# Kernel tuning notes

Hardware: AMD Instinct MI355X
Metric: run time of the kernel (lower is better)

Reference implementation:

```python
import jax, jax.numpy as jnp
import numpy as np

B, S, D_MODEL = 2, 2048, 768
N_QK, D_QK = 16, 16
N_OV, D_OV = 256, 1
VKV = 16
ROT_DIM, ROT_BASE = 16, 10000.0
SCALE = D_QK ** 0.5  # attn_scale defaults to sqrt(d_qk_head)


def _rotary_sin_cos(n_ctx, rotary_dim, base):
    # TransformerLens-style, non-adjacent pairs (GPT-NeoX)
    pos = jnp.arange(n_ctx, dtype=jnp.float32)
    dim = jnp.arange(rotary_dim // 2, dtype=jnp.float32)
    freq = base ** (dim / (rotary_dim / 2))
    freq = jnp.concatenate([freq, freq])  # 'd -> (2 d)'
    angles = pos[:, None] / freq[None, :]  # [n_ctx, rotary_dim]
    return jnp.sin(angles), jnp.cos(angles)


def _apply_rotary(x, sin, cos):
    # x: [B, S, H, d_head]; rotate first ROT_DIM dims, pass through the rest
    s = x.shape[1]
    xr = x[..., :ROT_DIM]
    half = ROT_DIM // 2
    rot = jnp.concatenate([-xr[..., half:], xr[..., :half]], axis=-1)  # rotate_every_two (non-adjacent)
    xr = xr * cos[:s, None, :] + rot * sin[:s, None, :]
    return jnp.concatenate([xr, x[..., ROT_DIM:]], axis=-1) if x.shape[-1] > ROT_DIM else xr


def setup_inputs() -> dict:
    key = jax.random.key(0)
    ks = jax.random.split(key, 6)
    std_qk = np.sqrt(2.0 / (D_MODEL * D_QK))   # kaiming fan_in for [H, d_model, d_head]
    std_v = np.sqrt(2.0 / (D_MODEL * D_OV))
    std_o = np.sqrt(2.0 / (D_OV * D_MODEL))
    std_vk = np.sqrt(2.0 / (N_QK * D_QK))
    return {
        "resid": jax.random.normal(ks[0], (B, S, D_MODEL), jnp.float32),
        "W_Q": jax.random.normal(ks[1], (N_QK, D_MODEL, D_QK), jnp.float32) * std_qk,
        "W_K": jax.random.normal(ks[2], (N_QK, D_MODEL, D_QK), jnp.float32) * std_qk,
        "W_V": jax.random.normal(ks[3], (N_OV, D_MODEL, D_OV), jnp.float32) * std_v,
        "W_O": jax.random.normal(ks[4], (N_OV, D_OV, D_MODEL), jnp.float32) * std_o,
        "b_Q": jnp.zeros((N_QK, D_QK), jnp.float32),
        "b_K": jnp.zeros((N_QK, D_QK), jnp.float32),
        "b_V": jnp.zeros((N_OV, D_OV), jnp.float32),
        "b_O": jnp.zeros((D_MODEL,), jnp.float32),
        "virtual_k": jax.random.normal(ks[5], (VKV, N_QK, D_QK), jnp.float32) * std_vk,
        "virtual_v": jnp.zeros((VKV, N_OV, D_OV), jnp.float32),
    }


def reference(resid, W_Q, W_K, W_V, W_O, b_Q, b_K, b_V, b_O, virtual_k, virtual_v):
    b, s, _ = resid.shape
    sin, cos = _rotary_sin_cos(s, ROT_DIM, ROT_BASE)

    q = jnp.einsum('bsd,hde->bshe', resid, W_Q) + b_Q  # [B,S,N_QK,D_QK]
    k = jnp.einsum('bsd,hde->bshe', resid, W_K) + b_K
    v = jnp.einsum('bsd,hde->bshe', resid, W_V) + b_V  # [B,S,N_OV,1]

    q = _apply_rotary(q, sin, cos)
    k = _apply_rotary(k, sin, cos)

    # append virtual KV along key axis
    k = jnp.concatenate([k, jnp.broadcast_to(virtual_k[None], (b, VKV, N_QK, D_QK))], axis=1)
    v = jnp.concatenate([v, jnp.broadcast_to(virtual_v[None], (b, VKV, N_OV, D_OV))], axis=1)

    scores = jnp.einsum('bqhe,bkhe->bhqk', q, k) / SCALE  # [B,H,S,S+VKV]
    i = jnp.arange(s)[:, None]
    j = jnp.arange(s + VKV)[None, :]
    mask = (j - i) <= VKV  # tril(.., diagonal=VKV)
    scores = jnp.where(mask, scores, -jnp.inf)
    pattern = jax.nn.softmax(scores, axis=-1)
    pattern = jnp.where(jnp.isnan(pattern), 0.0, pattern)

    r = N_OV // N_QK
    v_r = v.transpose(0, 2, 1, 3).reshape(b, N_QK, r, s + VKV, D_OV)  # [B,n_qk,r,K,1]
    z = jnp.einsum('bnqk,bnrkh->bnrqh', pattern, v_r)  # [B,n_qk,r,S,1]
    z = z.reshape(b, N_OV, s, D_OV).transpose(0, 2, 1, 3)  # [B,S,N_OV,1]

    out = jnp.einsum('bqhd,hdm->bqm', z, W_O) + b_O  # [B,S,D_MODEL]
    return out
```

## Files before the change

kernel.cpp:

```cpp
#include <hip/hip_runtime.h>
#include <hip/hip_bf16.h>
#include <math.h>

#define B_   2
#define S_   2048
#define DM   768
#define H_   16
#define C_   256
#define VKV_ 16
#define SK   2064
#define SKP  2080
#define NT_  65

#define TSPLIT 16
#define MAXSP  5
#define NACT   164

typedef __attribute__((ext_vector_type(8))) short short8;
typedef __attribute__((ext_vector_type(4))) short short4v;
typedef __attribute__((ext_vector_type(4))) float f32x4;
typedef __attribute__((ext_vector_type(16))) float f32x16;
typedef __attribute__((ext_vector_type(4))) unsigned uint4v;

#define QSCALE 0.360673760222240851f
#define L2B8   1.6609640474436811f

__device__ __forceinline__ short tobf(float f) {
    union { float f; unsigned u; } x; x.f = f;
    unsigned r = x.u + 0x7FFFu + ((x.u >> 16) & 1u);
    return (short)(r >> 16);
}
__device__ __forceinline__ float frombf_lo(unsigned u) {
    union { unsigned u; float f; } x; x.u = u << 16; return x.f;
}
__device__ __forceinline__ float frombf_hi(unsigned u) {
    union { unsigned u; float f; } x; x.u = u & 0xFFFF0000u; return x.f;
}

__device__ __forceinline__ void gload_lds16(const short* g, short* l) {
    __builtin_amdgcn_global_load_lds(
        (const __attribute__((address_space(1))) unsigned int*)g,
        (__attribute__((address_space(3))) unsigned int*)l, 16, 0, 0);
}

#define NRES (4096*768/4)
#define NWQ  (768*768)
#define NWO  (768*256)
__global__ __launch_bounds__(256) void conv_all(
    const float* __restrict__ resid,
    const float* __restrict__ WQ, const float* __restrict__ WK,
    const float* __restrict__ WV, const float* __restrict__ WO,
    const float* __restrict__ bQ, const float* __restrict__ bK,
    const float* __restrict__ bV,
    const float* __restrict__ vKp, const float* __restrict__ vVp,
    short* __restrict__ Ab, short* __restrict__ Wqkv_t,
    short* __restrict__ WtO, float* __restrict__ bqkv,
    short* __restrict__ Kb2, short* __restrict__ Vt3)
{
    int t = blockIdx.x * 256 + threadIdx.x;
    if (t < NRES) {
        float4 v = *(const float4*)(resid + (size_t)t * 4);
        short4v o = { tobf(v.x), tobf(v.y), tobf(v.z), tobf(v.w) };
        *(short4v*)(Ab + (size_t)t * 4) = o;
        return;
    }
    t -= NRES;
    if (t < NWQ) {
        int cc = t / 768, d = t % 768;
        float w;
        if (cc < 256)      w = WQ[((size_t)(cc >> 4) * DM + d) * 16 + (cc & 15)];
        else if (cc < 512) w = WK[((size_t)((cc - 256) >> 4) * DM + d) * 16 + (cc & 15)];
        else               w = WV[(size_t)(cc - 512) * DM + d];
        Wqkv_t[t] = tobf(w);
        return;
    }
    t -= NWQ;
    if (t < NWO) {
        int c = t & 255, m = t >> 8;
        WtO[t] = tobf(WO[(size_t)c * DM + m]);
        return;
    }
    t -= NWO;
    if (t < 768) {
        bqkv[t] = (t < 256) ? bQ[t] : (t < 512 ? bK[t - 256] : bV[t - 512]);
        return;
    }
    t -= 768;
    if (t < 32 * 32) {
        const int bh = t >> 5;
        const int s  = S_ + (t & 31);
        const int h  = bh & 15;
        short kb[16], vb[16];
        if (s < SK) {
            const int tt = s - S_;
#pragma unroll
            for (int e = 0; e < 16; ++e) {
                kb[e] = tobf(vKp[(size_t)tt * 256 + h * 16 + e]);
                vb[e] = tobf(vVp[(size_t)tt * 256 + h * 16 + e]);
            }
        } else {
#pragma unroll
            for (int e = 0; e < 16; ++e) { kb[e] = 0; vb[e] = 0; }
        }
        const int t5 = s >> 5;
        short* kbase = Kb2 + ((size_t)bh * NT_ + t5) * 512 + (s & 31) * 8;
#pragma unroll
        for (int e = 0; e < 8; ++e)  { kbase[e] = kb[e]; kbase[256 + e] = kb[e + 8]; }
        short* vbase = Vt3 + ((size_t)bh * NT_ + t5) * 1024
                     + ((s >> 4) & 1) * 512 + ((s >> 3) & 1) * 8 + (s & 7);
#pragma unroll
        for (int dv = 0; dv < 16; ++dv) vbase[dv * 16] = vb[dv];
    }
}

__global__ __launch_bounds__(256) void mm_qkv(
    const short* __restrict__ A, const short* __restrict__ Bt,
    const float* __restrict__ bias,
    short* __restrict__ Qb2, short* __restrict__ Kb2, short* __restrict__ Vt3)
{
    __shared__ short As[128 * 64];
    __shared__ short Bs[64 * 64];

    const int tid  = threadIdx.x;
    const int w    = tid >> 6;
    const int lane = tid & 63;
    const int wm   = w >> 1, wn = w & 1;
    const int g    = lane >> 4, c = lane & 15;
    const int m0   = blockIdx.y * 128;
    const int n0   = blockIdx.x * 64;

    f32x4 acc[4][2];
#pragma unroll
    for (int i = 0; i < 4; ++i)
#pragma unroll
        for (int j = 0; j < 2; ++j) acc[i][j] = (f32x4){0.f, 0.f, 0.f, 0.f};

    const int lr = lane >> 3;
    const int lc = lane & 7;

    for (int k0 = 0; k0 < 768; k0 += 64) {
#pragma unroll
        for (int i = 0; i < 4; ++i) {
            const int ch  = i * 4 + w;
            const int row = ch * 8 + lr;
            const int scc = lc ^ (row & 7);
            gload_lds16(A + (size_t)(m0 + row) * 768 + k0 + scc * 8, As + ch * 512);
        }
#pragma unroll
        for (int i = 0; i < 2; ++i) {
            const int ch  = i * 4 + w;
            const int row = ch * 8 + lr;
            const int scc = lc ^ (row & 7);
            gload_lds16(Bt + (size_t)(n0 + row) * 768 + k0 + scc * 8, Bs + ch * 512);
        }
        __syncthreads();
#pragma unroll
        for (int kk = 0; kk < 64; kk += 32) {
            short8 af[4], bf[2];
#pragma unroll
            for (int i = 0; i < 4; ++i) {
                const int row = wm * 64 + i * 16 + c;
                const int sc  = ((kk >> 3) + g) ^ (row & 7);
                af[i] = *(const short8*)(As + row * 64 + sc * 8);
            }
#pragma unroll
            for (int j = 0; j < 2; ++j) {
                const int row = wn * 32 + j * 16 + c;
                const int sc  = ((kk >> 3) + g) ^ (row & 7);
                bf[j] = *(const short8*)(Bs + row * 64 + sc * 8);
            }
#pragma unroll
            for (int i = 0; i < 4; ++i)
#pragma unroll
                for (int j = 0; j < 2; ++j)
                    acc[i][j] = __builtin_amdgcn_mfma_f32_16x16x32_bf16(
                        af[i], bf[j], acc[i][j], 0, 0, 0);
        }
        __syncthreads();
    }

    const float bv0 = bias[n0 + wn * 32 + c];
    const float bv1 = bias[n0 + wn * 32 + 16 + c];

    if (n0 < 512) {
        const int isQ = (n0 < 256) ? 1 : 0;
        const float invf = __builtin_amdgcn_exp2f(-(float)(c & 7) * L2B8);
        const int h0 = (((n0 + wn * 32) & 255) >> 4);
        const int elo = (c & 8) ? 0 : 1;
#pragma unroll
        for (int i = 0; i < 4; ++i) {
#pragma unroll
            for (int r = 0; r < 4; ++r) {
                const int row = m0 + wm * 64 + i * 16 + 4 * g + r;
                const int s   = row & 2047;
                const int b   = row >> 11;
                float sn, cs;
                __sincosf((float)s * invf, &sn, &cs);
#pragma unroll
                for (int j = 0; j < 2; ++j) {
                    float val = acc[i][j][r] + (j ? bv1 : bv0);
                    float par = __shfl_xor(val, 8);
                    float rot = elo ? -par : par;
                    float out = val * cs + rot * sn;
                    if (isQ) out *= QSCALE;
                    const int bh = b * 16 + h0 + j;
                    const size_t base = isQ
                        ? ((size_t)bh * 64 + (s >> 5)) * 512
                        : ((size_t)bh * NT_ + (s >> 5)) * 512;
                    short* dst = (isQ ? Qb2 : Kb2) + base
                               + (s & 31) * 8 + (c >> 3) * 256 + (c & 7);
                    *dst = tobf(out);
                }
            }
        }
    } else {
        const int h0 = ((n0 + wn * 32 - 512) >> 4);
#pragma unroll
        for (int i = 0; i < 4; ++i) {
#pragma unroll
            for (int r = 0; r < 4; ++r) {
                const int row = m0 + wm * 64 + i * 16 + 4 * g + r;
                const int s   = row & 2047;
                const int b   = row >> 11;
#pragma unroll
                for (int j = 0; j < 2; ++j) {
                    float val = acc[i][j][r] + (j ? bv1 : bv0);
                    const int bh = b * 16 + h0 + j;
                    short* dst = Vt3 + ((size_t)bh * NT_ + (s >> 5)) * 1024
                               + ((s >> 4) & 1) * 512 + ((s >> 3) & 1) * 8 + (s & 7)
                               + c * 16;
                    *dst = tobf(val);
                }
            }
        }
    }
}

__global__ __launch_bounds__(256) void mm_out(
    const short* __restrict__ A, const short* __restrict__ Bt,
    const float* __restrict__ bias, float* __restrict__ Cout)
{
    __shared__ short As[128 * 64];
    __shared__ short Bs[64 * 64];

    const int tid  = threadIdx.x;
    const int w    = tid >> 6;
    const int lane = tid & 63;
    const int wm   = w >> 1, wn = w & 1;
    const int g    = lane >> 4, c = lane & 15;
    const int m0   = blockIdx.y * 128;
    const int n0   = blockIdx.x * 64;

    f32x4 acc[4][2];
#pragma unroll
    for (int i = 0; i < 4; ++i)
#pragma unroll
        for (int j = 0; j < 2; ++j) acc[i][j] = (f32x4){0.f, 0.f, 0.f, 0.f};

    const int lr = lane >> 3;
    const int lc = lane & 7;

    for (int k0 = 0; k0 < 256; k0 += 64) {
#pragma unroll
        for (int i = 0; i < 4; ++i) {
            const int ch  = i * 4 + w;
            const int row = ch * 8 + lr;
            const int scc = lc ^ (row & 7);
            gload_lds16(A + (size_t)(m0 + row) * 256 + k0 + scc * 8, As + ch * 512);
        }
#pragma unroll
        for (int i = 0; i < 2; ++i) {
            const int ch  = i * 4 + w;
            const int row = ch * 8 + lr;
            const int scc = lc ^ (row & 7);
            gload_lds16(Bt + (size_t)(n0 + row) * 256 + k0 + scc * 8, Bs + ch * 512);
        }
        __syncthreads();
#pragma unroll
        for (int kk = 0; kk < 64; kk += 32) {
            short8 af[4], bf[2];
#pragma unroll
            for (int i = 0; i < 4; ++i) {
                const int row = wm * 64 + i * 16 + c;
                const int sc  = ((kk >> 3) + g) ^ (row & 7);
                af[i] = *(const short8*)(As + row * 64 + sc * 8);
            }
#pragma unroll
            for (int j = 0; j < 2; ++j) {
                const int row = wn * 32 + j * 16 + c;
                const int sc  = ((kk >> 3) + g) ^ (row & 7);
                bf[j] = *(const short8*)(Bs + row * 64 + sc * 8);
            }
#pragma unroll
            for (int i = 0; i < 4; ++i)
#pragma unroll
                for (int j = 0; j < 2; ++j)
                    acc[i][j] = __builtin_amdgcn_mfma_f32_16x16x32_bf16(
                        af[i], bf[j], acc[i][j], 0, 0, 0);
        }
        __syncthreads();
    }
#pragma unroll
    for (int i = 0; i < 4; ++i)
#pragma unroll
        for (int j = 0; j < 2; ++j) {
            const int col = n0 + wn * 32 + j * 16 + c;
            const float bv = bias[col];
#pragma unroll
            for (int r = 0; r < 4; ++r) {
                const int row = m0 + wm * 64 + i * 16 + 4 * g + r;
                Cout[(size_t)row * DM + col] = acc[i][j][r] + bv;
            }
        }
}

__global__ __launch_bounds__(256) void attn_split(
    const short* __restrict__ Qb2, const short* __restrict__ Kb2,
    const short* __restrict__ Vt3, unsigned* __restrict__ PartA,
    float* __restrict__ PartL)
{
    const int w    = threadIdx.x >> 6;
    const int lane = threadIdx.x & 63;
    const int blk  = blockIdx.x;
    const int xcd  = blk & 7;
    const int j    = blk >> 3;
    const int bhl  = j / 41;
    const int slot = j - bhl * 41;
    const int bh   = xcd * 4 + bhl;
    const int r    = slot * 4 + w;
    int qt, sp;
    if (r < 49)       { sp = 1; qt = 15 + r; }
    else if (r < 82)  { sp = 2; qt = 31 + (r - 49); }
    else if (r < 99)  { sp = 3; qt = 47 + (r - 82); }
    else if (r == 99) { sp = 4; qt = 63; }
    else              { sp = 0; qt = 163 - r; }

    const int nt   = qt + 2;
    const int t0   = sp * TSPLIT;
    const int tend = min(t0 + TSPLIT, nt);

    const int hi = lane >> 5;
    const int qc = lane & 31;
    const int q0 = qt * 32;

    const f32x16 zero16 = {0,0,0,0,0,0,0,0,0,0,0,0,0,0,0,0};

    short8 qf = *(const short8*)(Qb2 + ((size_t)bh * 64 + qt) * 512 + lane * 8);

    f32x16 acc = zero16;
    float lsum = 0.f;

    const short* kbase = Kb2 + (size_t)bh * NT_ * 512 + lane * 8;
    const short* vbase = Vt3 + (size_t)bh * NT_ * 1024 + (lane & 15) * 16 + hi * 8;
    const int qv16  = q0 + qc + 16;
    const int tmask = (q0 + 17) >> 5;

#define LK(tt)  (*(const short8*)(kbase + (size_t)(tt) * 512))
#define LVA(tt) (*(const short8*)(vbase + (size_t)(tt) * 1024))
#define LVB(tt) (*(const short8*)(vbase + (size_t)(tt) * 1024 + 512))

#define SOFTMAX_TILE(S, tt, B1, B2)                                          \
    {                                                                        \
        if ((tt) >= tmask) {                                                 \
            const int kt_ = (tt) * 32;                                       \
            _Pragma("unroll")                                                \
            for (int rr = 0; rr < 16; ++rr) {                                \
                const int key = kt_ + (rr & 3) + 8 * (rr >> 2) + 4 * hi;     \
                S[rr] = (key <= qv16) ? S[rr] : -INFINITY;                   \
            }                                                                \
        }                                                                    \
        unsigned pk[8];                                                      \
        _Pragma("unroll")                                                    \
        for (int jj = 0; jj < 8; ++jj) {                                     \
            const float p0 = __builtin_amdgcn_exp2f(S[2 * jj]);              \
            const float p1 = __builtin_amdgcn_exp2f(S[2 * jj + 1]);          \
            lsum += p0 + p1;                                                 \
            asm("v_cvt_pk_bf16_f32 %0, %1, %2" : "=v"(pk[jj]) : "v"(p0), "v"(p1)); \
        }                                                                    \
        unsigned a0 = pk[0], a2 = pk[2], a1 = pk[1], a3 = pk[3];             \
        unsigned a4 = pk[4], a6 = pk[6], a5 = pk[5], a7 = pk[7];             \
        asm("v_permlane32_swap_b32 %0, %1" : "+v"(a0), "+v"(a2));            \
        asm("v_permlane32_swap_b32 %0, %1" : "+v"(a1), "+v"(a3));            \
        asm("v_permlane32_swap_b32 %0, %1" : "+v"(a4), "+v"(a6));            \
        asm("v_permlane32_swap_b32 %0, %1" : "+v"(a5), "+v"(a7));            \
        B1.u[0] = a0; B1.u[1] = a1; B1.u[2] = a2; B1.u[3] = a3;              \
        B2.u[0] = a4; B2.u[1] = a5; B2.u[2] = a6; B2.u[3] = a7;              \
    }

    const int npair_end = t0 + ((tend - t0) & ~1);

    if (t0 < npair_end) {
        short8 kfA = LK(t0),     vaA = LVA(t0),     vvA = LVB(t0);
        short8 kfB = LK(t0 + 1), vaB = LVA(t0 + 1), vvB = LVB(t0 + 1);

        for (int t = t0; t < npair_end; t += 2) {
            short8 kfA_n = kfA, vaA_n = vaA, vvA_n = vvA;
            short8 kfB_n = kfB, vaB_n = vaB, vvB_n = vvB;
            if (t + 2 < npair_end) {
                kfA_n = LK(t + 2); vaA_n = LVA(t + 2); vvA_n = LVB(t + 2);
                kfB_n = LK(t + 3); vaB_n = LVA(t + 3); vvB_n = LVB(t + 3);
            }

            f32x16 S0 = __builtin_amdgcn_mfma_f32_32x32x16_bf16(kfA, qf, zero16, 0, 0, 0);
            f32x16 S1 = __builtin_amdgcn_mfma_f32_32x32x16_bf16(kfB, qf, zero16, 0, 0, 0);

            union { unsigned u[4]; short8 v; } b1A, b2A, b1B, b2B;
            SOFTMAX_TILE(S0, t,     b1A, b2A);
            SOFTMAX_TILE(S1, t + 1, b1B, b2B);

            acc = __builtin_amdgcn_mfma_f32_32x32x16_bf16(vaA, b1A.v, acc, 0, 0, 0);
            acc = __builtin_amdgcn_mfma_f32_32x32x16_bf16(vvA, b2A.v, acc, 0, 0, 0);
            acc = __builtin_amdgcn_mfma_f32_32x32x16_bf16(vaB, b1B.v, acc, 0, 0, 0);
            acc = __builtin_amdgcn_mfma_f32_32x32x16_bf16(vvB, b2B.v, acc, 0, 0, 0);

            kfA = kfA_n; vaA = vaA_n; vvA = vvA_n;
            kfB = kfB_n; vaB = vaB_n; vvB = vvB_n;
        }
    }
    if (npair_end < tend) {
        const int t = npair_end;
        short8 kf = LK(t), va = LVA(t), vv = LVB(t);
        f32x16 S0 = __builtin_amdgcn_mfma_f32_32x32x16_bf16(kf, qf, zero16, 0, 0, 0);
        union { unsigned u[4]; short8 v; } b1, b2;
        SOFTMAX_TILE(S0, t, b1, b2);
        acc = __builtin_amdgcn_mfma_f32_32x32x16_bf16(va, b1.v, acc, 0, 0, 0);
        acc = __builtin_amdgcn_mfma_f32_32x32x16_bf16(vv, b2.v, acc, 0, 0, 0);
    }

    uint4v pa;
    asm("v_cvt_pk_bf16_f32 %0, %1, %2" : "=v"(pa.x) : "v"(acc[0]), "v"(acc[1]));
    asm("v_cvt_pk_bf16_f32 %0, %1, %2" : "=v"(pa.y) : "v"(acc[2]), "v"(acc[3]));
    asm("v_cvt_pk_bf16_f32 %0, %1, %2" : "=v"(pa.z) : "v"(acc[4]), "v"(acc[5]));
    asm("v_cvt_pk_bf16_f32 %0, %1, %2" : "=v"(pa.w) : "v"(acc[6]), "v"(acc[7]));

    const int pidx = (bh * 64 + qt) * MAXSP + sp;
    *(uint4v*)(PartA + ((size_t)pidx * 64 + lane) * 4) = pa;

    lsum += __shfl_xor(lsum, 32);
    if (hi == 0) PartL[(size_t)pidx * 32 + qc] = lsum;
}

__global__ __launch_bounds__(256) void attn_combine(
    const unsigned* __restrict__ PartA, const float* __restrict__ PartL,
    short* __restrict__ Zb)
{
    const int w    = threadIdx.x >> 6;
    const int lane = threadIdx.x & 63;
    const int wid  = blockIdx.x * 4 + w;
    const int bh   = wid >> 6;
    const int qt   = wid & 63;
    const int hi   = lane >> 5;
    const int qc   = lane & 31;
    const int ns   = (qt + 2 + TSPLIT - 1) / TSPLIT;

    float a[8];
#pragma unroll
    for (int rr = 0; rr < 8; ++rr) a[rr] = 0.f;
    float lsum = 0.f;

    const int pbase = (bh * 64 + qt) * MAXSP;
    for (int sp = 0; sp < ns; ++sp) {
        uint4v pa = *(const uint4v*)(PartA + ((size_t)(pbase + sp) * 64 + lane) * 4);
        a[0] += frombf_lo(pa.x); a[1] += frombf_hi(pa.x);
        a[2] += frombf_lo(pa.y); a[3] += frombf_hi(pa.y);
        a[4] += frombf_lo(pa.z); a[5] += frombf_hi(pa.z);
        a[6] += frombf_lo(pa.w); a[7] += frombf_hi(pa.w);
        lsum += PartL[(size_t)(pbase + sp) * 32 + qc];
    }
    const float inv = 1.f / lsum;

    const int b = bh >> 4, h = bh & 15;
    const int q0 = qt * 32;
    short* zp = Zb + ((size_t)(b * S_ + q0 + qc)) * C_ + h * 16;
    unsigned o01, o23, o45, o67;
    {
        float a0 = a[0] * inv, a1 = a[1] * inv, a2 = a[2] * inv, a3 = a[3] * inv;
        float a4 = a[4] * inv, a5 = a[5] * inv, a6 = a[6] * inv, a7 = a[7] * inv;
        asm("v_cvt_pk_bf16_f32 %0, %1, %2" : "=v"(o01) : "v"(a0), "v"(a1));
        asm("v_cvt_pk_bf16_f32 %0, %1, %2" : "=v"(o23) : "v"(a2), "v"(a3));
        asm("v_cvt_pk_bf16_f32 %0, %1, %2" : "=v"(o45) : "v"(a4), "v"(a5));
        asm("v_cvt_pk_bf16_f32 %0, %1, %2" : "=v"(o67) : "v"(a6), "v"(a7));
    }
    *(unsigned*)(zp + 4 * hi)         = o01;
    *(unsigned*)(zp + 4 * hi + 2)     = o23;
    *(unsigned*)(zp + 8 + 4 * hi)     = o45;
    *(unsigned*)(zp + 8 + 4 * hi + 2) = o67;
}

extern "C" void kernel_launch(void* const* d_in, const int* in_sizes, int n_in,
                              void* d_out, int out_size, void* d_ws, size_t ws_size,
                              hipStream_t stream)
{
    const float* resid = (const float*)d_in[0];
    const float* WQ = (const float*)d_in[1];
    const float* WK = (const float*)d_in[2];
    const float* WV = (const float*)d_in[3];
    const float* WO = (const float*)d_in[4];
    const float* bQ = (const float*)d_in[5];
    const float* bK = (const float*)d_in[6];
    const float* bV = (const float*)d_in[7];
    const float* bO = (const float*)d_in[8];
    const float* vK = (const float*)d_in[9];
    const float* vV = (const float*)d_in[10];
    float* out = (float*)d_out;
    float* ws  = (float*)d_ws;

    short* Zb   = (short*)ws;
    float* bqkv = ws + 3145728;
    short* Ab   = (short*)(ws + 3145728 + 768);
    short* Wqt  = Ab + 3145728;
    short* WtO  = Wqt + 589824;
    short* Qb2  = WtO + 196608;
    short* Kb2  = Qb2 + 1048576;
    short* Vt3  = Kb2 + 1064960;
    unsigned* PartA = (unsigned*)(Vt3 + 2129920);
    float*    PartL = (float*)(PartA + 2621440);

    const int conv_total = NRES + NWQ + NWO + 768 + 1024;
    conv_all<<<dim3((conv_total + 255) / 256), 256, 0, stream>>>(
        resid, WQ, WK, WV, WO, bQ, bK, bV, vK, vV,
        Ab, Wqt, WtO, bqkv, Kb2, Vt3);
    mm_qkv<<<dim3(12, 32), 256, 0, stream>>>(Ab, Wqt, bqkv, Qb2, Kb2, Vt3);
    attn_split<<<dim3(32 * NACT / 4), 256, 0, stream>>>(Qb2, Kb2, Vt3, PartA, PartL);
    attn_combine<<<dim3(512), 256, 0, stream>>>(PartA, PartL, Zb);
    mm_out<<<dim3(12, 32), 256, 0, stream>>>(Zb, WtO, bO, out);
}
```

Measured before the change: 61.33 us.

## Fuse split-KV attention and combine into one kernel with shared LDS K/V staging

Measured after the change: 68.02 us. 10.9% more time.

```diff
diff --git a/kernel.cpp b/kernel.cpp
--- a/kernel.cpp
+++ b/kernel.cpp
@@ -12,15 +12,10 @@
 #define SKP  2080
 #define NT_  65
 
-#define TSPLIT 16
-#define MAXSP  5
-#define NACT   164
-
 typedef __attribute__((ext_vector_type(8))) short short8;
 typedef __attribute__((ext_vector_type(4))) short short4v;
 typedef __attribute__((ext_vector_type(4))) float f32x4;
 typedef __attribute__((ext_vector_type(16))) float f32x16;
-typedef __attribute__((ext_vector_type(4))) unsigned uint4v;
 
 #define QSCALE 0.360673760222240851f
 #define L2B8   1.6609640474436811f
@@ -29,12 +24,6 @@
     union { float f; unsigned u; } x; x.f = f;
     unsigned r = x.u + 0x7FFFu + ((x.u >> 16) & 1u);
     return (short)(r >> 16);
-}
-__device__ __forceinline__ float frombf_lo(unsigned u) {
-    union { unsigned u; float f; } x; x.u = u << 16; return x.f;
-}
-__device__ __forceinline__ float frombf_hi(unsigned u) {
-    union { unsigned u; float f; } x; x.u = u & 0xFFFF0000u; return x.f;
 }
 
 __device__ __forceinline__ void gload_lds16(const short* g, short* l) {
@@ -314,168 +303,116 @@
         }
 }
 
-__global__ __launch_bounds__(256) void attn_split(
+__global__ __launch_bounds__(256) void attn_fused(
     const short* __restrict__ Qb2, const short* __restrict__ Kb2,
-    const short* __restrict__ Vt3, unsigned* __restrict__ PartA,
-    float* __restrict__ PartL)
+    const short* __restrict__ Vt3, short* __restrict__ Zb)
 {
+    __shared__ short Ks[8][512];
+    __shared__ short Vs[8][1024];
+
     const int w    = threadIdx.x >> 6;
     const int lane = threadIdx.x & 63;
     const int blk  = blockIdx.x;
     const int xcd  = blk & 7;
     const int j    = blk >> 3;
-    const int bhl  = j / 41;
-    const int slot = j - bhl * 41;
+    const int bhl  = j >> 4;
+    const int g    = 15 - (j & 15);
     const int bh   = xcd * 4 + bhl;
-    const int r    = slot * 4 + w;
-    int qt, sp;
-    if (r < 49)       { sp = 1; qt = 15 + r; }
-    else if (r < 82)  { sp = 2; qt = 31 + (r - 49); }
-    else if (r < 99)  { sp = 3; qt = 47 + (r - 82); }
-    else if (r == 99) { sp = 4; qt = 63; }
-    else              { sp = 0; qt = 163 - r; }
-
-    const int nt   = qt + 2;
-    const int t0   = sp * TSPLIT;
-    const int tend = min(t0 + TSPLIT, nt);
+
+    const int qt    = 4 * g + w;
+    const int myNt  = qt + 2;
+    const int ntmax = 4 * g + 5;
 
     const int hi = lane >> 5;
     const int qc = lane & 31;
     const int q0 = qt * 32;
+    const int qv16  = q0 + qc + 16;
+    const int tmask = (q0 + 17) >> 5;
 
     const f32x16 zero16 = {0,0,0,0,0,0,0,0,0,0,0,0,0,0,0,0};
 
     short8 qf = *(const short8*)(Qb2 + ((size_t)bh * 64 + qt) * 512 + lane * 8);
+    asm volatile("s_waitcnt vmcnt(0)" ::: "memory");
+
+    const short* ktile = Kb2 + (size_t)bh * NT_ * 512 + lane * 8;
+    const short* vtile = Vt3 + (size_t)bh * NT_ * 1024 + lane * 8;
+    const int voffs = (lane & 15) * 16 + hi * 8;
 
     f32x16 acc = zero16;
     float lsum = 0.f;
 
-    const short* kbase = Kb2 + (size_t)bh * NT_ * 512 + lane * 8;
-    const short* vbase = Vt3 + (size_t)bh * NT_ * 1024 + (lane & 15) * 16 + hi * 8;
-    const int qv16  = q0 + qc + 16;
-    const int tmask = (q0 + 17) >> 5;
-
-#define LK(tt)  (*(const short8*)(kbase + (size_t)(tt) * 512))
-#define LVA(tt) (*(const short8*)(vbase + (size_t)(tt) * 1024))
-#define LVB(tt) (*(const short8*)(vbase + (size_t)(tt) * 1024 + 512))
-
-#define SOFTMAX_TILE(S, tt, B1, B2)                                          \
-    {                                                                        \
-        if ((tt) >= tmask) {                                                 \
-            const int kt_ = (tt) * 32;                                       \
-            _Pragma("unroll")                                                \
-            for (int rr = 0; rr < 16; ++rr) {                                \
-                const int key = kt_ + (rr & 3) + 8 * (rr >> 2) + 4 * hi;     \
-                S[rr] = (key <= qv16) ? S[rr] : -INFINITY;                   \
-            }                                                                \
-        }                                                                    \
-        unsigned pk[8];                                                      \
-        _Pragma("unroll")                                                    \
-        for (int jj = 0; jj < 8; ++jj) {                                     \
-            const float p0 = __builtin_amdgcn_exp2f(S[2 * jj]);              \
-            const float p1 = __builtin_amdgcn_exp2f(S[2 * jj + 1]);          \
-            lsum += p0 + p1;                                                 \
-            asm("v_cvt_pk_bf16_f32 %0, %1, %2" : "=v"(pk[jj]) : "v"(p0), "v"(p1)); \
-        }                                                                    \
-        unsigned a0 = pk[0], a2 = pk[2], a1 = pk[1], a3 = pk[3];             \
-        unsigned a4 = pk[4], a6 = pk[6], a5 = pk[5], a7 = pk[7];             \
-        asm("v_permlane32_swap_b32 %0, %1" : "+v"(a0), "+v"(a2));            \
-        asm("v_permlane32_swap_b32 %0, %1" : "+v"(a1), "+v"(a3));            \
-        asm("v_permlane32_swap_b32 %0, %1" : "+v"(a4), "+v"(a6));            \
-        asm("v_permlane32_swap_b32 %0, %1" : "+v"(a5), "+v"(a7));            \
-        B1.u[0] = a0; B1.u[1] = a1; B1.u[2] = a2; B1.u[3] = a3;              \
-        B2.u[0] = a4; B2.u[1] = a5; B2.u[2] = a6; B2.u[3] = a7;              \
-    }
-
-    const int npair_end = t0 + ((tend - t0) & ~1);
-
-    if (t0 < npair_end) {
-        short8 kfA = LK(t0),     vaA = LVA(t0),     vvA = LVB(t0);
-        short8 kfB = LK(t0 + 1), vaB = LVA(t0 + 1), vvB = LVB(t0 + 1);
-
-        for (int t = t0; t < npair_end; t += 2) {
-            short8 kfA_n = kfA, vaA_n = vaA, vvA_n = vvA;
-            short8 kfB_n = kfB, vaB_n = vaB, vvB_n = vvB;
-            if (t + 2 < npair_end) {
-                kfA_n = LK(t + 2); vaA_n = LVA(t + 2); vvA_n = LVB(t + 2);
-                kfB_n = LK(t + 3); vaB_n = LVA(t + 3); vvB_n = LVB(t + 3);
-            }
-
-            f32x16 S0 = __builtin_amdgcn_mfma_f32_32x32x16_bf16(kfA, qf, zero16, 0, 0, 0);
-            f32x16 S1 = __builtin_amdgcn_mfma_f32_32x32x16_bf16(kfB, qf, zero16, 0, 0, 0);
-
-            union { unsigned u[4]; short8 v; } b1A, b2A, b1B, b2B;
-            SOFTMAX_TILE(S0, t,     b1A, b2A);
-            SOFTMAX_TILE(S1, t + 1, b1B, b2B);
-
-            acc = __builtin_amdgcn_mfma_f32_32x32x16_bf16(vaA, b1A.v, acc, 0, 0, 0);
-            acc = __builtin_amdgcn_mfma_f32_32x32x16_bf16(vvA, b2A.v, acc, 0, 0, 0);
-            acc = __builtin_amdgcn_mfma_f32_32x32x16_bf16(vaB, b1B.v, acc, 0, 0, 0);
-            acc = __builtin_amdgcn_mfma_f32_32x32x16_bf16(vvB, b2B.v, acc, 0, 0, 0);
-
-            kfA = kfA_n; vaA = vaA_n; vvA = vvA_n;
-            kfB = kfB_n; vaB = vaB_n; vvB = vvB_n;
-        }
-    }
-    if (npair_end < tend) {
-        const int t = npair_end;
-        short8 kf = LK(t), va = LVA(t), vv = LVB(t);
-        f32x16 S0 = __builtin_amdgcn_mfma_f32_32x32x16_bf16(kf, qf, zero16, 0, 0, 0);
-        union { unsigned u[4]; short8 v; } b1, b2;
-        SOFTMAX_TILE(S0, t, b1, b2);
-        acc = __builtin_amdgcn_mfma_f32_32x32x16_bf16(va, b1.v, acc, 0, 0, 0);
-        acc = __builtin_amdgcn_mfma_f32_32x32x16_bf16(vv, b2.v, acc, 0, 0, 0);
-    }
-
-    uint4v pa;
-    asm("v_cvt_pk_bf16_f32 %0, %1, %2" : "=v"(pa.x) : "v"(acc[0]), "v"(acc[1]));
-    asm("v_cvt_pk_bf16_f32 %0, %1, %2" : "=v"(pa.y) : "v"(acc[2]), "v"(acc[3]));
-    asm("v_cvt_pk_bf16_f32 %0, %1, %2" : "=v"(pa.z) : "v"(acc[4]), "v"(acc[5]));
-    asm("v_cvt_pk_bf16_f32 %0, %1, %2" : "=v"(pa.w) : "v"(acc[6]), "v"(acc[7]));
-
-    const int pidx = (bh * 64 + qt) * MAXSP + sp;
-    *(uint4v*)(PartA + ((size_t)pidx * 64 + lane) * 4) = pa;
+#define STAGE(tt) do {                                                        \
+        if (w == 0)      gload_lds16(ktile + (size_t)(tt) * 512,  &Ks[(tt) & 7][0]);   \
+        else if (w == 1) gload_lds16(vtile + (size_t)(tt) * 1024, &Vs[(tt) & 7][0]);   \
+        else if (w == 2) gload_lds16(vtile + (size_t)(tt) * 1024 + 512, &Vs[(tt) & 7][512]); \
+    } while (0)
+
+#define COMPUTE(tt) do {                                                      \
+        if ((tt) < myNt) {                                                    \
+            short8 kf = *(const short8*)(&Ks[(tt) & 7][lane * 8]);            \
+            short8 va = *(const short8*)(&Vs[(tt) & 7][voffs]);               \
+            short8 vv = *(const short8*)(&Vs[(tt) & 7][512 + voffs]);         \
+            f32x16 S = __builtin_amdgcn_mfma_f32_32x32x16_bf16(kf, qf, zero16, 0, 0, 0); \
+            if ((tt) >= tmask) {                                              \
+                const int kt_ = (tt) * 32;                                    \
+                _Pragma("unroll")                                             \
+                for (int rr = 0; rr < 16; ++rr) {                             \
+                    const int key = kt_ + (rr & 3) + 8 * (rr >> 2) + 4 * hi;  \
+                    S[rr] = (key <= qv16) ? S[rr] : -INFINITY;                \
+                }                                                             \
+            }                                                                 \
+            unsigned pk[8];                                                   \
+            _Pragma("unroll")                                                 \
+            for (int jj = 0; jj < 8; ++jj) {                                  \
+                const float p0 = __builtin_amdgcn_exp2f(S[2 * jj]);           \
+                const float p1 = __builtin_amdgcn_exp2f(S[2 * jj + 1]);       \
+                lsum += p0 + p1;                                              \
+                asm("v_cvt_pk_bf16_f32 %0, %1, %2" : "=v"(pk[jj]) : "v"(p0), "v"(p1)); \
+            }                                                                 \
+            unsigned a0 = pk[0], a2 = pk[2], a1 = pk[1], a3 = pk[3];          \
+            unsigned a4 = pk[4], a6 = pk[6], a5 = pk[5], a7 = pk[7];          \
+            asm("v_permlane32_swap_b32 %0, %1" : "+v"(a0), "+v"(a2));         \
+            asm("v_permlane32_swap_b32 %0, %1" : "+v"(a1), "+v"(a3));         \
+            asm("v_permlane32_swap_b32 %0, %1" : "+v"(a4), "+v"(a6));         \
+            asm("v_permlane32_swap_b32 %0, %1" : "+v"(a5), "+v"(a7));         \
+            union { unsigned u[4]; short8 v; } b1, b2;                        \
+            b1.u[0] = a0; b1.u[1] = a1; b1.u[2] = a2; b1.u[3] = a3;           \
+            b2.u[0] = a4; b2.u[1] = a5; b2.u[2] = a6; b2.u[3] = a7;           \
+            acc = __builtin_amdgcn_mfma_f32_32x32x16_bf16(va, b1.v, acc, 0, 0, 0); \
+            acc = __builtin_amdgcn_mfma_f32_32x32x16_bf16(vv, b2.v, acc, 0, 0, 0); \
+        }                                                                     \
+    } while (0)
+
+    STAGE(0); STAGE(1); STAGE(2); STAGE(3); STAGE(4);
+
+    for (int t = 0; t + 5 < ntmax; ++t) {
+        STAGE(t + 5);
+        asm volatile("s_waitcnt vmcnt(5)" ::: "memory");
+        __builtin_amdgcn_s_barrier();
+        __builtin_amdgcn_sched_barrier(0);
+        COMPUTE(t);
+    }
+#define EPI(kk, cnt) {                                                        \
+        const int t = ntmax - 5 + (kk);                                       \
+        asm volatile("s_waitcnt vmcnt(" #cnt ")" ::: "memory");               \
+        __builtin_amdgcn_s_barrier();                                         \
+        __builtin_amdgcn_sched_barrier(0);                                    \
+        COMPUTE(t);                                                           \
+    }
+    EPI(0, 4) EPI(1, 3) EPI(2, 2) EPI(3, 1) EPI(4, 0)
+#undef EPI
+#undef COMPUTE
+#undef STAGE
 
     lsum += __shfl_xor(lsum, 32);
-    if (hi == 0) PartL[(size_t)pidx * 32 + qc] = lsum;
-}
-
-__global__ __launch_bounds__(256) void attn_combine(
-    const unsigned* __restrict__ PartA, const float* __restrict__ PartL,
-    short* __restrict__ Zb)
-{
-    const int w    = threadIdx.x >> 6;
-    const int lane = threadIdx.x & 63;
-    const int wid  = blockIdx.x * 4 + w;
-    const int bh   = wid >> 6;
-    const int qt   = wid & 63;
-    const int hi   = lane >> 5;
-    const int qc   = lane & 31;
-    const int ns   = (qt + 2 + TSPLIT - 1) / TSPLIT;
-
-    float a[8];
-#pragma unroll
-    for (int rr = 0; rr < 8; ++rr) a[rr] = 0.f;
-    float lsum = 0.f;
-
-    const int pbase = (bh * 64 + qt) * MAXSP;
-    for (int sp = 0; sp < ns; ++sp) {
-        uint4v pa = *(const uint4v*)(PartA + ((size_t)(pbase + sp) * 64 + lane) * 4);
-        a[0] += frombf_lo(pa.x); a[1] += frombf_hi(pa.x);
-        a[2] += frombf_lo(pa.y); a[3] += frombf_hi(pa.y);
-        a[4] += frombf_lo(pa.z); a[5] += frombf_hi(pa.z);
-        a[6] += frombf_lo(pa.w); a[7] += frombf_hi(pa.w);
-        lsum += PartL[(size_t)(pbase + sp) * 32 + qc];
-    }
     const float inv = 1.f / lsum;
 
     const int b = bh >> 4, h = bh & 15;
-    const int q0 = qt * 32;
     short* zp = Zb + ((size_t)(b * S_ + q0 + qc)) * C_ + h * 16;
     unsigned o01, o23, o45, o67;
     {
-        float a0 = a[0] * inv, a1 = a[1] * inv, a2 = a[2] * inv, a3 = a[3] * inv;
-        float a4 = a[4] * inv, a5 = a[5] * inv, a6 = a[6] * inv, a7 = a[7] * inv;
+        float a0 = acc[0] * inv, a1 = acc[1] * inv, a2 = acc[2] * inv, a3 = acc[3] * inv;
+        float a4 = acc[4] * inv, a5 = acc[5] * inv, a6 = acc[6] * inv, a7 = acc[7] * inv;
         asm("v_cvt_pk_bf16_f32 %0, %1, %2" : "=v"(o01) : "v"(a0), "v"(a1));
         asm("v_cvt_pk_bf16_f32 %0, %1, %2" : "=v"(o23) : "v"(a2), "v"(a3));
         asm("v_cvt_pk_bf16_f32 %0, %1, %2" : "=v"(o45) : "v"(a4), "v"(a5));
@@ -513,15 +450,12 @@
     short* Qb2  = WtO + 196608;
     short* Kb2  = Qb2 + 1048576;
     short* Vt3  = Kb2 + 1064960;
-    unsigned* PartA = (unsigned*)(Vt3 + 2129920);
-    float*    PartL = (float*)(PartA + 2621440);
 
     const int conv_total = NRES + NWQ + NWO + 768 + 1024;
     conv_all<<<dim3((conv_total + 255) / 256), 256, 0, stream>>>(
         resid, WQ, WK, WV, WO, bQ, bK, bV, vK, vV,
         Ab, Wqt, WtO, bqkv, Kb2, Vt3);
     mm_qkv<<<dim3(12, 32), 256, 0, stream>>>(Ab, Wqt, bqkv, Qb2, Kb2, Vt3);
-    attn_split<<<dim3(32 * NACT / 4), 256, 0, stream>>>(Qb2, Kb2, Vt3, PartA, PartL);
-    attn_combine<<<dim3(512), 256, 0, stream>>>(PartA, PartL, Zb);
+    attn_fused<<<dim3(512), 256, 0, stream>>>(Qb2, Kb2, Vt3, Zb);
     mm_out<<<dim3(12, 32), 256, 0, stream>>>(Zb, WtO, bO, out);
 }
```
